# Kernel tuning notes

Hardware: AMD Instinct MI355X
Metric: run time of the kernel (lower is better)

The kernel has to match this reference:

```python
import jax, jax.numpy as jnp
import numpy as np


def _combos(n, k):
    # all n-tuples of nonnegative ints summing to k, same order as the torch module
    if n == 1:
        yield (k,)
        return
    for i in range(k + 1):
        for t in _combos(n - 1, k - i):
            yield (i,) + t


def _make_exponents(action_dim, rank):
    rows = []
    for total in range(rank + 1):
        rows.extend(_combos(action_dim, total))
    # [action_dim, num_basis], matching the registered buffer exponents.T layout
    return np.asarray(rows, dtype=np.int32).T


def setup_inputs() -> dict:
    key = jax.random.key(0)
    action_dim, rank, batch = 8, 4, 131072
    actions = jax.random.normal(key, (batch, action_dim), dtype=jnp.float32)
    exponents = jnp.asarray(_make_exponents(action_dim, rank))  # [D, NB], NB=495
    return {"actions": actions, "exponents": exponents, "rank": rank}


def reference(actions, exponents, rank):
    # actions: [B, D] float; exponents: [D, NB] int32; rank: python int
    x = jnp.clip(actions, -1.0, 1.0)  # [B, D]
    # Legendre recurrence P_n(x) = ((2n-1)/n) x P_{n-1}(x) - ((n-1)/n) P_{n-2}(x)
    polys = [jnp.ones_like(x)]
    if rank >= 1:
        polys.append(x)
    for n in range(2, rank + 1):
        polys.append(((2.0 * n - 1.0) / n) * x * polys[-1] - ((n - 1.0) / n) * polys[-2])
    P = jnp.stack(polys, axis=-1)  # [B, D, rank+1]
    # gather the needed order per (dimension, basis function) and multiply over dims
    idx = jnp.broadcast_to(exponents[None, :, :], (x.shape[0],) + exponents.shape)  # [B, D, NB]
    gathered = jnp.take_along_axis(P, idx.astype(jnp.int32), axis=2)  # [B, D, NB]
    return jnp.prod(gathered, axis=1)  # [B, NB]
```

## Files before the change

### kernel.cpp

```cpp
#include <hip/hip_runtime.h>
#include <math.h>


#define THREADS 256
#define TILE 16
#define ROWSTRIDE 41

__global__ __launch_bounds__(THREADS, 8) void legendre_fast(
    const float* __restrict__ actions,
    const int* __restrict__ exps,
    float* __restrict__ out,
    int B, int D, int NB, int rank, int rows_per_block)
{
    __shared__ unsigned prog[1024];
    __shared__ float Pl[TILE * ROWSTRIDE];

    const int t = threadIdx.x;

    for (int nb = t; nb < NB; nb += THREADS) {
        unsigned pk = 0;
        int shift = 0;
        for (int d = 0; d < D; ++d) {
            int e = exps[d * NB + nb];
            if (e > 0) {
                pk |= (unsigned)(d * 5 + e) << shift;
                shift += 6;
            }
        }
        prog[nb] = pk;
    }

    int r0 = blockIdx.x * rows_per_block;
    int rend = r0 + rows_per_block;
    if (rend > B) rend = B;

    for (; r0 < rend; r0 += TILE) {
        int nrows = rend - r0;
        if (nrows > TILE) nrows = TILE;

        if (t < nrows * D) {
            int rl = t / D;
            int d  = t - rl * D;
            float x = actions[(long long)(r0 + rl) * D + d];
            x = fminf(fmaxf(x, -1.0f), 1.0f);
            float* Pr = &Pl[rl * ROWSTRIDE + d * 5];
            float p0 = 1.0f, p1 = x;
            Pr[0] = 1.0f;
            if (rank >= 1) Pr[1] = x;
            for (int n = 2; n <= rank; ++n) {
                float fn = (float)n;
                float pn = ((2.0f * fn - 1.0f) / fn) * x * p1
                         - ((fn - 1.0f) / fn) * p0;
                Pr[n] = pn;
                p0 = p1;
                p1 = pn;
            }
        }
        __syncthreads();

        int total_o = nrows * NB;
        long long gbase = (long long)r0 * NB;
        int rl = t / NB;
        int nb = t - rl * NB;
        for (int o = t; o < total_o; o += THREADS) {
            unsigned pk = prog[nb];
            const float* Pr = &Pl[rl * ROWSTRIDE];
            float f0 = Pr[pk & 63u];
            float f1 = Pr[(pk >> 6) & 63u];
            float f2 = Pr[(pk >> 12) & 63u];
            float f3 = Pr[(pk >> 18) & 63u];
            out[gbase + o] = (f0 * f1) * (f2 * f3);
            nb += THREADS;
            while (nb >= NB) { nb -= NB; ++rl; }
        }
        __syncthreads();
    }
}

__global__ void legendre_generic(
    const float* __restrict__ actions,
    const int* __restrict__ exps,
    float* __restrict__ out,
    long long total, int D, int NB)
{
    long long stride = (long long)gridDim.x * blockDim.x;
    for (long long i = (long long)blockIdx.x * blockDim.x + threadIdx.x;
         i < total; i += stride) {
        int nb = (int)(i % NB);
        long long row = i / NB;
        float prod = 1.0f;
        for (int d = 0; d < D; ++d) {
            int e = exps[d * NB + nb];
            float x = actions[row * D + d];
            x = fminf(fmaxf(x, -1.0f), 1.0f);
            float p0 = 1.0f, p1 = x;
            float p = (e == 0) ? 1.0f : x;
            for (int n = 2; n <= e; ++n) {
                float fn = (float)n;
                float pn = ((2.0f * fn - 1.0f) / fn) * x * p1
                         - ((fn - 1.0f) / fn) * p0;
                p0 = p1;
                p1 = pn;
                p = pn;
            }
            prod *= p;
        }
        out[i] = prod;
    }
}

extern "C" void kernel_launch(void* const* d_in, const int* in_sizes, int n_in,
                              void* d_out, int out_size, void* d_ws, size_t ws_size,
                              hipStream_t stream) {
    const float* actions = (const float*)d_in[0];
    const int* exps = (const int*)d_in[1];
    float* out = (float*)d_out;

    long long in0 = in_sizes[0];
    long long in1 = in_sizes[1];
    long long osz = out_size;

    int D = (int)(sqrt((double)in0 * (double)in1 / (double)osz) + 0.5);
    if (D < 1) D = 1;
    int NB = (int)(in1 / D);
    int B = (int)(in0 / D);

    int rank = -1;
    {
        long long c = 1;
        for (int r = 0; r <= 32; ++r) {
            if (c == (long long)NB) { rank = r; break; }
            c = c * (D + r + 1) / (r + 1);
            if (c > (long long)NB) break;
        }
    }

    bool fast = (rank >= 0 && rank <= 4 && D >= 1 && D <= 8 &&
                 NB >= 1 && NB <= 1024 && (long long)B * NB == osz &&
                 (long long)B * D == in0);

    if (fast) {
        int nblk = 2048;
        if (B < nblk) nblk = B;
        int rpb = (B + nblk - 1) / nblk;
        legendre_fast<<<nblk, THREADS, 0, stream>>>(
            actions, exps, out, B, D, NB, rank, rpb);
    } else {
        long long total = osz;
        long long want = (total + 255) / 256;
        int nblk = (want > 8192) ? 8192 : (int)(want > 0 ? want : 1);
        legendre_generic<<<nblk, 256, 0, stream>>>(
            actions, exps, out, total, D, NB);
    }
}
```

Measured before the change: 57.35 us.

## Vectorize output stores to float4 nontemporal, one tile per block

Each block now handles exactly one 32-row tile, launching B/32 blocks instead of 2048 blocks that loop over tiles. Each thread computes four consecutive outputs and writes them as a single 16-byte nontemporal store, replacing scalar stores. The basis-program table in shared memory is stored in an interleaved layout to reduce bank conflicts. The trade-off is that every block rebuilds the program table, and the fast path now requires B divisible by 32 and NB of at most 512.

```diff
diff --git a/kernel.cpp b/kernel.cpp
--- a/kernel.cpp
+++ b/kernel.cpp
@@ -3,19 +3,22 @@
 
 
 #define THREADS 256
-#define TILE 16
+#define TILE 32
 #define ROWSTRIDE 41
+
+typedef float f32x4 __attribute__((ext_vector_type(4)));
 
 __global__ __launch_bounds__(THREADS, 8) void legendre_fast(
     const float* __restrict__ actions,
     const int* __restrict__ exps,
     float* __restrict__ out,
-    int B, int D, int NB, int rank, int rows_per_block)
+    int B, int D, int NB, int rank, int stepq, int stepr)
 {
-    __shared__ unsigned prog[1024];
+    __shared__ unsigned prog[512];
     __shared__ float Pl[TILE * ROWSTRIDE];
 
     const int t = threadIdx.x;
+    const int r0 = blockIdx.x * TILE;
 
     for (int nb = t; nb < NB; nb += THREADS) {
         unsigned pk = 0;
@@ -27,53 +30,58 @@
                 shift += 6;
             }
         }
-        prog[nb] = pk;
+        prog[((nb & 3) << 7) | (nb >> 2)] = pk;
     }
 
-    int r0 = blockIdx.x * rows_per_block;
-    int rend = r0 + rows_per_block;
-    if (rend > B) rend = B;
+    if (t < TILE * D) {
+        int rl = t / D;
+        int d  = t - rl * D;
+        float x = actions[(long long)(r0 + rl) * D + d];
+        x = fminf(fmaxf(x, -1.0f), 1.0f);
+        float* Pr = &Pl[rl * ROWSTRIDE + d * 5];
+        float p0 = 1.0f, p1 = x;
+        Pr[0] = 1.0f;
+        if (rank >= 1) Pr[1] = x;
+        for (int n = 2; n <= rank; ++n) {
+            float fn = (float)n;
+            float pn = ((2.0f * fn - 1.0f) / fn) * x * p1
+                     - ((fn - 1.0f) / fn) * p0;
+            Pr[n] = pn;
+            p0 = p1;
+            p1 = pn;
+        }
+    }
+    __syncthreads();
 
-    for (; r0 < rend; r0 += TILE) {
-        int nrows = rend - r0;
-        if (nrows > TILE) nrows = TILE;
+    const int nchunks = (TILE * NB) >> 2;
+    f32x4* __restrict__ o4 = (f32x4*)(out + (long long)r0 * NB);
 
-        if (t < nrows * D) {
-            int rl = t / D;
-            int d  = t - rl * D;
-            float x = actions[(long long)(r0 + rl) * D + d];
-            x = fminf(fmaxf(x, -1.0f), 1.0f);
-            float* Pr = &Pl[rl * ROWSTRIDE + d * 5];
-            float p0 = 1.0f, p1 = x;
-            Pr[0] = 1.0f;
-            if (rank >= 1) Pr[1] = x;
-            for (int n = 2; n <= rank; ++n) {
-                float fn = (float)n;
-                float pn = ((2.0f * fn - 1.0f) / fn) * x * p1
-                         - ((fn - 1.0f) / fn) * p0;
-                Pr[n] = pn;
-                p0 = p1;
-                p1 = pn;
-            }
-        }
-        __syncthreads();
+    int o0 = t << 2;
+    int rl = o0 / NB;
+    int nb = o0 - rl * NB;
 
-        int total_o = nrows * NB;
-        long long gbase = (long long)r0 * NB;
-        int rl = t / NB;
-        int nb = t - rl * NB;
-        for (int o = t; o < total_o; o += THREADS) {
-            unsigned pk = prog[nb];
-            const float* Pr = &Pl[rl * ROWSTRIDE];
+    for (int c = t; c < nchunks; c += THREADS) {
+        int nbi = nb, rli = rl;
+        float res[4];
+#pragma unroll
+        for (int i = 0; i < 4; ++i) {
+            unsigned pk = prog[((nbi & 3) << 7) | (nbi >> 2)];
+            const float* Pr = &Pl[rli * ROWSTRIDE];
             float f0 = Pr[pk & 63u];
             float f1 = Pr[(pk >> 6) & 63u];
             float f2 = Pr[(pk >> 12) & 63u];
             float f3 = Pr[(pk >> 18) & 63u];
-            out[gbase + o] = (f0 * f1) * (f2 * f3);
-            nb += THREADS;
-            while (nb >= NB) { nb -= NB; ++rl; }
+            res[i] = (f0 * f1) * (f2 * f3);
+            ++nbi;
+            if (nbi == NB) { nbi = 0; ++rli; }
         }
-        __syncthreads();
+        f32x4 v;
+        v.x = res[0]; v.y = res[1]; v.z = res[2]; v.w = res[3];
+        __builtin_nontemporal_store(v, o4 + c);
+
+        nb += stepr;
+        rl += stepq;
+        if (nb >= NB) { nb -= NB; ++rl; }
     }
 }
 
@@ -136,15 +144,16 @@
     }
 
     bool fast = (rank >= 0 && rank <= 4 && D >= 1 && D <= 8 &&
-                 NB >= 1 && NB <= 1024 && (long long)B * NB == osz &&
-                 (long long)B * D == in0);
+                 NB >= 1 && NB <= 512 &&
+                 (long long)B * NB == osz && (long long)B * D == in0 &&
+                 (B % TILE) == 0 && ((TILE * NB) % 4) == 0);
 
     if (fast) {
-        int nblk = 2048;
-        if (B < nblk) nblk = B;
-        int rpb = (B + nblk - 1) / nblk;
+        int nblk = B / TILE;
+        int stepq = (THREADS * 4) / NB;
+        int stepr = (THREADS * 4) % NB;
         legendre_fast<<<nblk, THREADS, 0, stream>>>(
-            actions, exps, out, B, D, NB, rank, rpb);
+            actions, exps, out, B, D, NB, rank, stepq, stepr);
     } else {
         long long total = osz;
         long long want = (total + 255) / 256;
```

Result: faster. 55.42 us (-3.4%).
